# Performance work log

Hardware: AMD Instinct MI355X
Metric: run time of the kernel (lower is better)

Reference implementation:

```python
import jax, jax.numpy as jnp
import numpy as np

B_, S_, H_, O_ = 4, 2048, 2048, 2048
E_, R_ = 8, 16
LORA_ALPHA = 16.0


def setup_inputs() -> dict:
    key = jax.random.key(0)
    ks = jax.random.split(key, 5)
    x = jax.random.normal(ks[0], (B_, S_, H_), dtype=jnp.float32)
    W = jax.random.normal(ks[1], (O_, H_), dtype=jnp.float32) * 0.02   # frozen base weight [out, in]
    gate_w = jax.random.normal(ks[2], (E_, H_), dtype=jnp.float32) * 0.02  # router Linear weight [E, H]
    A = jax.random.normal(ks[3], (E_, R_, H_), dtype=jnp.float32) * 0.02   # stacked lora_A weights [E, r, in]
    B = jax.random.normal(ks[4], (E_, O_, R_), dtype=jnp.float32) * 0.02   # stacked lora_B weights [E, out, r]
    return {"x": x, "W": W, "gate_w": gate_w, "A": A, "B": B}


def reference(x, W, gate_w, A, B):
    bsz, seq, hid = x.shape
    E = gate_w.shape[0]
    x_flat = x.reshape(-1, hid)                                  # [T, H]

    # base linear
    out = x_flat @ W.T                                           # [T, O]

    # learned router: softmax -> top-2 -> renormalize
    logits = x_flat @ gate_w.T                                   # [T, E]
    probs = jax.nn.softmax(logits, axis=-1)
    topk_w, topk_idx = jax.lax.top_k(probs, 2)                   # [T, 2]
    topk_w = topk_w / jnp.sum(topk_w, axis=-1, keepdims=True)

    # per-token per-expert combine weight (sum over the 2 slots), scaled by alpha
    onehot = jax.nn.one_hot(topk_idx, E, dtype=x.dtype)          # [T, 2, E]
    wmat = jnp.einsum('tk,tke->te', topk_w, onehot) * LORA_ALPHA # [T, E]

    # dense grouped LoRA: h_e = x A_e^T ; out += sum_e w_te * (h_e B_e^T)
    h = jnp.einsum('th,erh->etr', x_flat, A)                     # [E, T, r]
    hw = h * wmat.T[:, :, None]                                  # [E, T, r]
    lora = jnp.einsum('etr,eor->to', hw, B)                      # [T, O]

    return (out + lora).reshape(bsz, seq, -1)
```

## Files before the change

### kernel.cpp

```cpp
#include <hip/hip_runtime.h>
#include <hip/hip_bf16.h>
#include <stdint.h>

#define T_TOK 8192
#define HID   2048
#define OUTD  2048
#define NE    8
#define RR    16
#define KAUG  2176
#define NH    128

typedef __bf16 bf16x8 __attribute__((ext_vector_type(8)));
typedef float  f32x4  __attribute__((ext_vector_type(4)));

#define AS1(p) ((__attribute__((address_space(1))) void*)(p))
#define AS3(p) ((__attribute__((address_space(3))) void*)(p))

__device__ inline unsigned short f2bf(float f) {
  unsigned int u = __builtin_bit_cast(unsigned int, f);
  unsigned int r = (u + 0x7fffu + ((u >> 16) & 1u)) >> 16;
  return (unsigned short)r;
}

__device__ inline ushort4 f2bf4(float4 v) {
  ushort4 u;
  u.x = f2bf(v.x); u.y = f2bf(v.y); u.z = f2bf(v.z); u.w = f2bf(v.w);
  return u;
}

__global__ __launch_bounds__(512) void k_prep(const float* __restrict__ x,
                                              const float* __restrict__ gw,
                                              const float* __restrict__ W,
                                              const float* __restrict__ Bw,
                                              const float* __restrict__ A,
                                              unsigned short* __restrict__ Xa,
                                              float* __restrict__ wte,
                                              unsigned short* __restrict__ Wa,
                                              unsigned short* __restrict__ Ag) {
  __shared__ float gws[NE * HID];
  if (blockIdx.x < 1024) {
#pragma unroll
    for (int i = 0; i < 8; ++i) {
      int idx = (i * 512 + (int)threadIdx.x) * 4;
      *(float4*)(gws + idx) = *(const float4*)(gw + idx);
    }
    __syncthreads();
    int w = threadIdx.x >> 6, lane = threadIdx.x & 63;
    int t = blockIdx.x * 8 + w;
    const float* xt = x + (size_t)t * HID;
    unsigned short* xo = Xa + (size_t)t * KAUG;
    double acc[8] = {0, 0, 0, 0, 0, 0, 0, 0};
#pragma unroll
    for (int i = 0; i < 8; ++i) {
      int k = (i * 64 + lane) * 4;
      float4 xv = *(const float4*)(xt + k);
      *(ushort4*)(xo + k) = f2bf4(xv);
#pragma unroll
      for (int e = 0; e < 8; ++e) {
        float4 gv = *(const float4*)(gws + e * HID + k);
        acc[e] += (double)xv.x * gv.x + (double)xv.y * gv.y +
                  (double)xv.z * gv.z + (double)xv.w * gv.w;
      }
    }
#pragma unroll
    for (int off = 32; off >= 1; off >>= 1)
#pragma unroll
      for (int e = 0; e < 8; ++e)
        acc[e] += __shfl_down(acc[e], off, 64);
    if (lane == 0) {
      int e0 = 0; double l0 = acc[0];
#pragma unroll
      for (int e = 1; e < 8; ++e) if (acc[e] > l0) { l0 = acc[e]; e0 = e; }
      int e1 = -1; double l1 = -1e300;
#pragma unroll
      for (int e = 0; e < 8; ++e) if (e != e0 && acc[e] > l1) { l1 = acc[e]; e1 = e; }
      double w0 = 16.0 / (1.0 + exp(l1 - l0));
      float o[8] = {0.f, 0.f, 0.f, 0.f, 0.f, 0.f, 0.f, 0.f};
      o[e0] = (float)w0;
      o[e1] = (float)(16.0 - w0);
      float4* p = (float4*)(wte + (size_t)t * 8);
      p[0] = make_float4(o[0], o[1], o[2], o[3]);
      p[1] = make_float4(o[4], o[5], o[6], o[7]);
    }
  } else {
    int b2 = blockIdx.x - 1024;
    if (b2 < 2048) {
      int tid = b2 * 512 + threadIdx.x;
      int row = tid >> 9, c = (tid & 511) << 2;
      float4 v = *(const float4*)(W + (size_t)row * HID + c);
      *(ushort4*)(Wa + (size_t)row * KAUG + c) = f2bf4(v);
    } else if (b2 < 2176) {
      int tid = (b2 - 2048) * 512 + threadIdx.x;
      int o = tid >> 5, j = (tid & 31) << 2;
      int e = j >> 4, r = j & 15;
      float4 v = *(const float4*)(Bw + (size_t)e * OUTD * RR + (size_t)o * RR + r);
      *(ushort4*)(Wa + (size_t)o * KAUG + 2048 + j) = f2bf4(v);
    } else {
      int tid = (b2 - 2176) * 512 + threadIdx.x;
      float4 v = *(const float4*)(A + (size_t)tid * 4);
      *(ushort4*)(Ag + (size_t)tid * 4) = f2bf4(v);
    }
  }
}

__global__ __launch_bounds__(256) void k_ha(const unsigned short* __restrict__ Xa,
                                            const unsigned short* __restrict__ Ag,
                                            const float* __restrict__ wte,
                                            unsigned short* __restrict__ XaW) {
  __shared__ unsigned short Xs[4][32 * 64];
  __shared__ unsigned short As[4][64 * 64];
  int tm = (blockIdx.x >> 1) * 32;
  int ch = (blockIdx.x & 1) * 64;
  int w = threadIdx.x >> 6, lane = threadIdx.x & 63;
  int lrow = lane >> 3;
  int lcol_s = (lane & 7) << 3;
  int lcol_g = ((lane & 7) ^ (lrow & 7)) << 3;

  const unsigned short* gX = Xa + (size_t)(tm + w * 8 + lrow) * KAUG + lcol_g;
  const unsigned short* gA = Ag + (size_t)(ch + w * 16 + lrow) * HID + lcol_g;
  int sxo = (w * 8 + lrow) * 64 + lcol_s;
  int sao = (w * 16 + lrow) * 64 + lcol_s;

  f32x4 acc[2] = {};

#define HA_STAGE(slot, koff) do {                                                         \
    __builtin_amdgcn_global_load_lds(AS1(gX + (koff)), AS3(&Xs[slot][0] + sxo), 16, 0, 0);\
    __builtin_amdgcn_global_load_lds(AS1(gA + (koff)), AS3(&As[slot][0] + sao), 16, 0, 0);\
    __builtin_amdgcn_global_load_lds(AS1(gA + (size_t)8 * HID + (koff)),                  \
                                     AS3(&As[slot][0] + 8 * 64 + sao), 16, 0, 0);         \
  } while (0)

#define HA_COMP(s) do {                                                                   \
    _Pragma("unroll")                                                                     \
    for (int ks = 0; ks < 2; ++ks) {                                                      \
      int kch = ks * 4 + (lane >> 4);                                                     \
      int ko = ((kch ^ (lane & 7)) << 3);                       \
      bf16x8 a = *(const bf16x8*)(&Xs[s][0] + ((w >> 1) * 16 + (lane & 15)) * 64 + ko);   \
      _Pragma("unroll")                                                                   \
      for (int fn = 0; fn < 2; ++fn) {                                                    \
        bf16x8 bv = *(const bf16x8*)(&As[s][0] + ((w & 1) * 32 + fn * 16 + (lane & 15)) * 64 + ko); \
        acc[fn] = __builtin_amdgcn_mfma_f32_16x16x32_bf16(a, bv, acc[fn], 0, 0, 0);       \
      }                                                                                   \
    }                                                                                     \
  } while (0)

  HA_STAGE(0, 0);
  HA_STAGE(1, 64);
  HA_STAGE(2, 128);
  for (int t = 0; t < 29; ++t) {
    asm volatile("s_waitcnt vmcnt(6)" ::: "memory");
    __builtin_amdgcn_s_barrier();
    HA_COMP(t & 3);
    __builtin_amdgcn_s_barrier();
    HA_STAGE((t + 3) & 3, (t + 3) * 64);
  }
  asm volatile("s_waitcnt vmcnt(6)" ::: "memory");
  __builtin_amdgcn_s_barrier();
  HA_COMP(1);
  asm volatile("s_waitcnt vmcnt(3)" ::: "memory");
  __builtin_amdgcn_s_barrier();
  HA_COMP(2);
  asm volatile("s_waitcnt vmcnt(0)" ::: "memory");
  __builtin_amdgcn_s_barrier();
  HA_COMP(3);
#undef HA_STAGE
#undef HA_COMP

  int q = lane >> 4;
#pragma unroll
  for (int fn = 0; fn < 2; ++fn) {
    int col = ch + (w & 1) * 32 + fn * 16 + (lane & 15);
    int e = col >> 4;
#pragma unroll
    for (int r = 0; r < 4; ++r) {
      int t = tm + (w >> 1) * 16 + q * 4 + r;
      float we = wte[(size_t)t * 8 + e];
      XaW[(size_t)t * KAUG + 2048 + col] = f2bf(we * acc[fn][r]);
    }
  }
}

__global__ __launch_bounds__(256, 4) void k_gemm(const unsigned short* __restrict__ Xa,
                                                 const unsigned short* __restrict__ Wa,
                                                 float* __restrict__ out) {
  __shared__ unsigned short As[128 * 64];
  __shared__ unsigned short Bs[128 * 64];
  int lid = blockIdx.x;
  int xcd = lid & 7, s = lid >> 3;
  int bm = (xcd * 8 + (s & 7)) * 128;
  int bn = (s >> 3) * 128;
  int w = threadIdx.x >> 6, lane = threadIdx.x & 63;
  int wm = (w >> 1) * 64, wn = (w & 1) * 64;
  int lrow = lane >> 3;
  int lcol_s = (lane & 7) << 3;
  int lcol_g = ((lane & 7) ^ (lrow & 7)) << 3;

  const unsigned short* gA = Xa + (size_t)(bm + w * 32 + lrow) * KAUG + lcol_g;
  const unsigned short* gB = Wa + (size_t)(bn + w * 32 + lrow) * KAUG + lcol_g;
  unsigned short* sA = As + (w * 32 + lrow) * 64 + lcol_s;
  unsigned short* sB = Bs + (w * 32 + lrow) * 64 + lcol_s;

  f32x4 acc[4][4] = {};
  for (int kt = 0; kt < KAUG; kt += 64) {
#pragma unroll
    for (int i = 0; i < 4; ++i) {
      __builtin_amdgcn_global_load_lds(AS1(gA + (size_t)i * 8 * KAUG), AS3(sA + i * 8 * 64), 16, 0, 0);
      __builtin_amdgcn_global_load_lds(AS1(gB + (size_t)i * 8 * KAUG), AS3(sB + i * 8 * 64), 16, 0, 0);
    }
    __syncthreads();
#pragma unroll
    for (int ks = 0; ks < 2; ++ks) {
      int kch = ks * 4 + (lane >> 4);
      int ko = ((kch ^ (lane & 7)) << 3);
      bf16x8 a[4], b[4];
#pragma unroll
      for (int f = 0; f < 4; ++f) a[f] = *(const bf16x8*)(As + (wm + f * 16 + (lane & 15)) * 64 + ko);
#pragma unroll
      for (int f = 0; f < 4; ++f) b[f] = *(const bf16x8*)(Bs + (wn + f * 16 + (lane & 15)) * 64 + ko);
#pragma unroll
      for (int fm = 0; fm < 4; ++fm)
#pragma unroll
        for (int fn = 0; fn < 4; ++fn)
          acc[fm][fn] = __builtin_amdgcn_mfma_f32_16x16x32_bf16(a[fm], b[fn], acc[fm][fn], 0, 0, 0);
    }
    __syncthreads();
    gA += 64; gB += 64;
  }
#pragma unroll
  for (int fm = 0; fm < 4; ++fm) {
    int row = bm + wm + fm * 16 + ((lane >> 4) << 2);
#pragma unroll
    for (int r = 0; r < 4; ++r) {
      float* orow = out + (size_t)(row + r) * OUTD + bn + wn + (lane & 15);
#pragma unroll
      for (int fn = 0; fn < 4; ++fn) orow[fn * 16] = acc[fm][fn][r];
    }
  }
}

extern "C" void kernel_launch(void* const* d_in, const int* in_sizes, int n_in,
                              void* d_out, int out_size, void* d_ws, size_t ws_size,
                              hipStream_t stream) {
  const float* x  = (const float*)d_in[0];
  const float* W  = (const float*)d_in[1];
  const float* gw = (const float*)d_in[2];
  const float* A  = (const float*)d_in[3];
  const float* B  = (const float*)d_in[4];
  float* out = (float*)d_out;

  char* ws = (char*)d_ws;
  unsigned short* Xa  = (unsigned short*)(ws);
  unsigned short* Wa  = (unsigned short*)(ws + 35651584);
  unsigned short* Ag  = (unsigned short*)(ws + 44564480);
  float*          wte = (float*)        (ws + 45088768);

  k_prep<<<3328, 512, 0, stream>>>(x, gw, W, B, A, Xa, wte, Wa, Ag);
  k_ha  <<<512, 256, 0, stream>>>(Xa, Ag, wte, Xa);
  k_gemm<<<1024, 256, 0, stream>>>(Xa, Wa, out);
}
```

Before: 220.7 us.

## Move weight conversion into k_ha and widen its blocks to cover all LoRA columns

The W and B fp32-to-bf16 conversion blocks move out of k_prep and into k_ha as extra blocks, so the weight conversion runs alongside the LoRA-A projection instead of before it. k_ha now uses 512-thread blocks that each compute all 128 expert-rank columns for a 32-token tile. This halves the number of times the X tile is loaded and drops the duplicated X loads. The per-wave vmcnt waits are adjusted because only four of the eight waves load X. The cost is more LDS per block and a larger, mixed-role grid for k_ha.

```diff
diff --git a/kernel.cpp b/kernel.cpp
--- a/kernel.cpp
+++ b/kernel.cpp
@@ -30,12 +30,9 @@
 
 __global__ __launch_bounds__(512) void k_prep(const float* __restrict__ x,
                                               const float* __restrict__ gw,
-                                              const float* __restrict__ W,
-                                              const float* __restrict__ Bw,
                                               const float* __restrict__ A,
                                               unsigned short* __restrict__ Xa,
                                               float* __restrict__ wte,
-                                              unsigned short* __restrict__ Wa,
                                               unsigned short* __restrict__ Ag) {
   __shared__ float gws[NE * HID];
   if (blockIdx.x < 1024) {
@@ -83,81 +80,91 @@
       p[1] = make_float4(o[4], o[5], o[6], o[7]);
     }
   } else {
-    int b2 = blockIdx.x - 1024;
+    int tid = (blockIdx.x - 1024) * 512 + threadIdx.x;
+    float4 v = *(const float4*)(A + (size_t)tid * 4);
+    *(ushort4*)(Ag + (size_t)tid * 4) = f2bf4(v);
+  }
+}
+
+__global__ __launch_bounds__(512) void k_ha(const unsigned short* __restrict__ Xa,
+                                            const unsigned short* __restrict__ Ag,
+                                            const float* __restrict__ wte,
+                                            unsigned short* __restrict__ XaW,
+                                            const float* __restrict__ W,
+                                            const float* __restrict__ Bw,
+                                            unsigned short* __restrict__ Wa) {
+  __shared__ unsigned short Xs[4][32 * 64];
+  __shared__ unsigned short As[4][128 * 64];
+  if (blockIdx.x >= 256) {
+    int b2 = blockIdx.x - 256;
     if (b2 < 2048) {
       int tid = b2 * 512 + threadIdx.x;
       int row = tid >> 9, c = (tid & 511) << 2;
       float4 v = *(const float4*)(W + (size_t)row * HID + c);
       *(ushort4*)(Wa + (size_t)row * KAUG + c) = f2bf4(v);
-    } else if (b2 < 2176) {
+    } else {
       int tid = (b2 - 2048) * 512 + threadIdx.x;
       int o = tid >> 5, j = (tid & 31) << 2;
       int e = j >> 4, r = j & 15;
       float4 v = *(const float4*)(Bw + (size_t)e * OUTD * RR + (size_t)o * RR + r);
       *(ushort4*)(Wa + (size_t)o * KAUG + 2048 + j) = f2bf4(v);
-    } else {
-      int tid = (b2 - 2176) * 512 + threadIdx.x;
-      float4 v = *(const float4*)(A + (size_t)tid * 4);
-      *(ushort4*)(Ag + (size_t)tid * 4) = f2bf4(v);
-    }
-  }
-}
-
-__global__ __launch_bounds__(256) void k_ha(const unsigned short* __restrict__ Xa,
-                                            const unsigned short* __restrict__ Ag,
-                                            const float* __restrict__ wte,
-                                            unsigned short* __restrict__ XaW) {
-  __shared__ unsigned short Xs[4][32 * 64];
-  __shared__ unsigned short As[4][64 * 64];
-  int tm = (blockIdx.x >> 1) * 32;
-  int ch = (blockIdx.x & 1) * 64;
+    }
+    return;
+  }
+
+  int tm = blockIdx.x * 32;
   int w = threadIdx.x >> 6, lane = threadIdx.x & 63;
+  int wm = (w >> 2) * 16, wn = (w & 3) * 32;
   int lrow = lane >> 3;
   int lcol_s = (lane & 7) << 3;
   int lcol_g = ((lane & 7) ^ (lrow & 7)) << 3;
 
-  const unsigned short* gX = Xa + (size_t)(tm + w * 8 + lrow) * KAUG + lcol_g;
-  const unsigned short* gA = Ag + (size_t)(ch + w * 16 + lrow) * HID + lcol_g;
-  int sxo = (w * 8 + lrow) * 64 + lcol_s;
+  const unsigned short* gX = Xa + (size_t)(tm + (w & 3) * 8 + lrow) * KAUG + lcol_g;
+  const unsigned short* gA = Ag + (size_t)(w * 16 + lrow) * HID + lcol_g;
+  int sxo = ((w & 3) * 8 + lrow) * 64 + lcol_s;
   int sao = (w * 16 + lrow) * 64 + lcol_s;
 
   f32x4 acc[2] = {};
 
-#define HA_STAGE(slot, koff) do {                                                         \
-    __builtin_amdgcn_global_load_lds(AS1(gX + (koff)), AS3(&Xs[slot][0] + sxo), 16, 0, 0);\
-    __builtin_amdgcn_global_load_lds(AS1(gA + (koff)), AS3(&As[slot][0] + sao), 16, 0, 0);\
-    __builtin_amdgcn_global_load_lds(AS1(gA + (size_t)8 * HID + (koff)),                  \
-                                     AS3(&As[slot][0] + 8 * 64 + sao), 16, 0, 0);         \
+#define HA_STAGE(slot, koff) do {                                                           \
+    if (w < 4)                                                                              \
+      __builtin_amdgcn_global_load_lds(AS1(gX + (koff)), AS3(&Xs[slot][0] + sxo), 16, 0, 0);\
+    __builtin_amdgcn_global_load_lds(AS1(gA + (koff)), AS3(&As[slot][0] + sao), 16, 0, 0);  \
+    __builtin_amdgcn_global_load_lds(AS1(gA + (size_t)8 * HID + (koff)),                    \
+                                     AS3(&As[slot][0] + 8 * 64 + sao), 16, 0, 0);           \
   } while (0)
 
-#define HA_COMP(s) do {                                                                   \
-    _Pragma("unroll")                                                                     \
-    for (int ks = 0; ks < 2; ++ks) {                                                      \
-      int kch = ks * 4 + (lane >> 4);                                                     \
-      int ko = ((kch ^ (lane & 7)) << 3);                       \
-      bf16x8 a = *(const bf16x8*)(&Xs[s][0] + ((w >> 1) * 16 + (lane & 15)) * 64 + ko);   \
-      _Pragma("unroll")                                                                   \
-      for (int fn = 0; fn < 2; ++fn) {                                                    \
-        bf16x8 bv = *(const bf16x8*)(&As[s][0] + ((w & 1) * 32 + fn * 16 + (lane & 15)) * 64 + ko); \
-        acc[fn] = __builtin_amdgcn_mfma_f32_16x16x32_bf16(a, bv, acc[fn], 0, 0, 0);       \
-      }                                                                                   \
-    }                                                                                     \
+#define HA_COMP(s) do {                                                                     \
+    _Pragma("unroll")                                                                       \
+    for (int ks = 0; ks < 2; ++ks) {                                                        \
+      int kch = ks * 4 + (lane >> 4);                                                       \
+      int ko = ((kch ^ (lane & 7)) << 3);                         \
+      bf16x8 a = *(const bf16x8*)(&Xs[s][0] + (wm + (lane & 15)) * 64 + ko);                \
+      _Pragma("unroll")                                                                     \
+      for (int fn = 0; fn < 2; ++fn) {                                                      \
+        bf16x8 bv = *(const bf16x8*)(&As[s][0] + (wn + fn * 16 + (lane & 15)) * 64 + ko);   \
+        acc[fn] = __builtin_amdgcn_mfma_f32_16x16x32_bf16(a, bv, acc[fn], 0, 0, 0);         \
+      }                                                                                     \
+    }                                                                                       \
   } while (0)
 
   HA_STAGE(0, 0);
   HA_STAGE(1, 64);
   HA_STAGE(2, 128);
   for (int t = 0; t < 29; ++t) {
-    asm volatile("s_waitcnt vmcnt(6)" ::: "memory");
+    if (w < 4) asm volatile("s_waitcnt vmcnt(6)" ::: "memory");
+    else       asm volatile("s_waitcnt vmcnt(4)" ::: "memory");
     __builtin_amdgcn_s_barrier();
     HA_COMP(t & 3);
     __builtin_amdgcn_s_barrier();
     HA_STAGE((t + 3) & 3, (t + 3) * 64);
   }
-  asm volatile("s_waitcnt vmcnt(6)" ::: "memory");
+  if (w < 4) asm volatile("s_waitcnt vmcnt(6)" ::: "memory");
+  else       asm volatile("s_waitcnt vmcnt(4)" ::: "memory");
   __builtin_amdgcn_s_barrier();
   HA_COMP(1);
-  asm volatile("s_waitcnt vmcnt(3)" ::: "memory");
+  if (w < 4) asm volatile("s_waitcnt vmcnt(3)" ::: "memory");
+  else       asm volatile("s_waitcnt vmcnt(2)" ::: "memory");
   __builtin_amdgcn_s_barrier();
   HA_COMP(2);
   asm volatile("s_waitcnt vmcnt(0)" ::: "memory");
@@ -169,11 +176,11 @@
   int q = lane >> 4;
 #pragma unroll
   for (int fn = 0; fn < 2; ++fn) {
-    int col = ch + (w & 1) * 32 + fn * 16 + (lane & 15);
+    int col = wn + fn * 16 + (lane & 15);
     int e = col >> 4;
 #pragma unroll
     for (int r = 0; r < 4; ++r) {
-      int t = tm + (w >> 1) * 16 + q * 4 + r;
+      int t = tm + wm + q * 4 + r;
       float we = wte[(size_t)t * 8 + e];
       XaW[(size_t)t * KAUG + 2048 + col] = f2bf(we * acc[fn][r]);
     }
@@ -254,7 +261,7 @@
   unsigned short* Ag  = (unsigned short*)(ws + 44564480);
   float*          wte = (float*)        (ws + 45088768);
 
-  k_prep<<<3328, 512, 0, stream>>>(x, gw, W, B, A, Xa, wte, Wa, Ag);
-  k_ha  <<<512, 256, 0, stream>>>(Xa, Ag, wte, Xa);
+  k_prep<<<1152, 512, 0, stream>>>(x, gw, A, Xa, wte, Ag);
+  k_ha  <<<2432, 512, 0, stream>>>(Xa, Ag, wte, Xa, W, B, Wa);
   k_gemm<<<1024, 256, 0, stream>>>(Xa, Wa, out);
 }
```

Result: slower. 227.4 us (+3.0%).

## Use 256x256 double-buffered GEMM tile with 512 threads and MFMA priority

Applied to the files above, without the earlier changes.

Replaces the 128x128 single-buffered main GEMM with a 256x256 tile computed by 8 waves, each owning a 128x64 sub-tile. LDS is double-buffered, so global-to-LDS loads for the next K-step run while the current step computes. s_setprio is raised around the MFMA blocks. The goal is more operand reuse per byte loaded and hidden load latency. The cost is 128 KB of LDS and 128 accumulator registers per lane, which limits occupancy to one block per CU, and the grid shrinks to 256 blocks.

```diff
diff --git a/kernel.cpp b/kernel.cpp
--- a/kernel.cpp
+++ b/kernel.cpp
@@ -9,6 +9,7 @@
 #define RR    16
 #define KAUG  2176
 #define NH    128
+#define NKT   34
 
 typedef __bf16 bf16x8 __attribute__((ext_vector_type(8)));
 typedef float  f32x4  __attribute__((ext_vector_type(4)));
@@ -134,7 +135,7 @@
     _Pragma("unroll")                                                                     \
     for (int ks = 0; ks < 2; ++ks) {                                                      \
       int kch = ks * 4 + (lane >> 4);                                                     \
-      int ko = ((kch ^ (lane & 7)) << 3);                       \
+      int ko = ((kch ^ (lane & 7)) << 3);                                                 \
       bf16x8 a = *(const bf16x8*)(&Xs[s][0] + ((w >> 1) * 16 + (lane & 15)) * 64 + ko);   \
       _Pragma("unroll")                                                                   \
       for (int fn = 0; fn < 2; ++fn) {                                                    \
@@ -180,60 +181,91 @@
   }
 }
 
-__global__ __launch_bounds__(256, 4) void k_gemm(const unsigned short* __restrict__ Xa,
+__global__ __launch_bounds__(512) void k_gemm256(const unsigned short* __restrict__ Xa,
                                                  const unsigned short* __restrict__ Wa,
                                                  float* __restrict__ out) {
-  __shared__ unsigned short As[128 * 64];
-  __shared__ unsigned short Bs[128 * 64];
-  int lid = blockIdx.x;
-  int xcd = lid & 7, s = lid >> 3;
-  int bm = (xcd * 8 + (s & 7)) * 128;
-  int bn = (s >> 3) * 128;
+  __shared__ unsigned short Asl[2][256 * 64];
+  __shared__ unsigned short Bsl[2][256 * 64];
+  int bid = blockIdx.x;
+  int xcd = bid & 7, idx = bid >> 3;
+  int bm = (xcd * 4 + (idx >> 3)) * 256;
+  int bn = (idx & 7) * 256;
   int w = threadIdx.x >> 6, lane = threadIdx.x & 63;
-  int wm = (w >> 1) * 64, wn = (w & 1) * 64;
+  int wm = (w >> 2) * 128;
+  int wn = (w & 3) * 64;
   int lrow = lane >> 3;
   int lcol_s = (lane & 7) << 3;
   int lcol_g = ((lane & 7) ^ (lrow & 7)) << 3;
 
-  const unsigned short* gA = Xa + (size_t)(bm + w * 32 + lrow) * KAUG + lcol_g;
-  const unsigned short* gB = Wa + (size_t)(bn + w * 32 + lrow) * KAUG + lcol_g;
-  unsigned short* sA = As + (w * 32 + lrow) * 64 + lcol_s;
-  unsigned short* sB = Bs + (w * 32 + lrow) * 64 + lcol_s;
-
-  f32x4 acc[4][4] = {};
-  for (int kt = 0; kt < KAUG; kt += 64) {
-#pragma unroll
-    for (int i = 0; i < 4; ++i) {
-      __builtin_amdgcn_global_load_lds(AS1(gA + (size_t)i * 8 * KAUG), AS3(sA + i * 8 * 64), 16, 0, 0);
-      __builtin_amdgcn_global_load_lds(AS1(gB + (size_t)i * 8 * KAUG), AS3(sB + i * 8 * 64), 16, 0, 0);
-    }
-    __syncthreads();
-#pragma unroll
-    for (int ks = 0; ks < 2; ++ks) {
-      int kch = ks * 4 + (lane >> 4);
-      int ko = ((kch ^ (lane & 7)) << 3);
-      bf16x8 a[4], b[4];
-#pragma unroll
-      for (int f = 0; f < 4; ++f) a[f] = *(const bf16x8*)(As + (wm + f * 16 + (lane & 15)) * 64 + ko);
-#pragma unroll
-      for (int f = 0; f < 4; ++f) b[f] = *(const bf16x8*)(Bs + (wn + f * 16 + (lane & 15)) * 64 + ko);
-#pragma unroll
-      for (int fm = 0; fm < 4; ++fm)
-#pragma unroll
-        for (int fn = 0; fn < 4; ++fn)
-          acc[fm][fn] = __builtin_amdgcn_mfma_f32_16x16x32_bf16(a[fm], b[fn], acc[fm][fn], 0, 0, 0);
-    }
-    __syncthreads();
-    gA += 64; gB += 64;
-  }
-#pragma unroll
-  for (int fm = 0; fm < 4; ++fm) {
-    int row = bm + wm + fm * 16 + ((lane >> 4) << 2);
+  const unsigned short* gA = Xa + (size_t)(bm + w * 8 + lrow) * KAUG + lcol_g;
+  const unsigned short* gB = Wa + (size_t)(bn + w * 8 + lrow) * KAUG + lcol_g;
+  int sO = (w * 8 + lrow) * 64 + lcol_s;
+
+#define G_STAGE(p, kt) do {                                                        \
+    _Pragma("unroll")                                                              \
+    for (int i = 0; i < 4; ++i) {                                                  \
+      __builtin_amdgcn_global_load_lds(AS1(gA + (size_t)i * 64 * KAUG + (kt) * 64),\
+                                       AS3(&Asl[p][0] + sO + i * 64 * 64), 16, 0, 0); \
+      __builtin_amdgcn_global_load_lds(AS1(gB + (size_t)i * 64 * KAUG + (kt) * 64),\
+                                       AS3(&Bsl[p][0] + sO + i * 64 * 64), 16, 0, 0); \
+    }                                                                              \
+  } while (0)
+
+  f32x4 acc[8][4] = {};
+
+#define G_COMP(p) do {                                                             \
+    __builtin_amdgcn_s_setprio(1);                                                 \
+    _Pragma("unroll")                                                              \
+    for (int kk = 0; kk < 2; ++kk) {                                               \
+      int kch = kk * 4 + (lane >> 4);                                              \
+      int ko = ((kch ^ (lane & 7)) << 3);                                          \
+      bf16x8 b[4];                                                                 \
+      _Pragma("unroll")                                                            \
+      for (int n = 0; n < 4; ++n)                                                  \
+        b[n] = *(const bf16x8*)(&Bsl[p][0] + (wn + n * 16 + (lane & 15)) * 64 + ko); \
+      _Pragma("unroll")                                                            \
+      for (int f = 0; f < 8; ++f) {                                                \
+        bf16x8 a = *(const bf16x8*)(&Asl[p][0] + (wm + f * 16 + (lane & 15)) * 64 + ko); \
+        _Pragma("unroll")                                                          \
+        for (int n = 0; n < 4; ++n)                                                \
+          acc[f][n] = __builtin_amdgcn_mfma_f32_16x16x32_bf16(a, b[n], acc[f][n], 0, 0, 0); \
+      }                                                                            \
+    }                                                                              \
+    __builtin_amdgcn_s_setprio(0);                                                 \
+  } while (0)
+
+  G_STAGE(0, 0);
+  G_STAGE(1, 1);
+  for (int kt = 0; kt < 32; kt += 2) {
+    asm volatile("s_waitcnt vmcnt(8)" ::: "memory");
+    __builtin_amdgcn_s_barrier();
+    G_COMP(0);
+    __builtin_amdgcn_s_barrier();
+    if (kt + 2 < NKT) G_STAGE(0, kt + 2);
+    asm volatile("s_waitcnt vmcnt(8)" ::: "memory");
+    __builtin_amdgcn_s_barrier();
+    G_COMP(1);
+    __builtin_amdgcn_s_barrier();
+    if (kt + 3 < NKT) G_STAGE(1, kt + 3);
+  }
+  asm volatile("s_waitcnt vmcnt(8)" ::: "memory");
+  __builtin_amdgcn_s_barrier();
+  G_COMP(0);
+  __builtin_amdgcn_s_barrier();
+  asm volatile("s_waitcnt vmcnt(0)" ::: "memory");
+  __builtin_amdgcn_s_barrier();
+  G_COMP(1);
+#undef G_STAGE
+#undef G_COMP
+
+#pragma unroll
+  for (int f = 0; f < 8; ++f) {
+    int row = bm + wm + f * 16 + ((lane >> 4) << 2);
 #pragma unroll
     for (int r = 0; r < 4; ++r) {
       float* orow = out + (size_t)(row + r) * OUTD + bn + wn + (lane & 15);
 #pragma unroll
-      for (int fn = 0; fn < 4; ++fn) orow[fn * 16] = acc[fm][fn][r];
+      for (int n = 0; n < 4; ++n) orow[n * 16] = acc[f][n][r];
     }
   }
 }
@@ -254,7 +286,7 @@
   unsigned short* Ag  = (unsigned short*)(ws + 44564480);
   float*          wte = (float*)        (ws + 45088768);
 
-  k_prep<<<3328, 512, 0, stream>>>(x, gw, W, B, A, Xa, wte, Wa, Ag);
-  k_ha  <<<512, 256, 0, stream>>>(Xa, Ag, wte, Xa);
-  k_gemm<<<1024, 256, 0, stream>>>(Xa, Wa, out);
-}
+  k_prep   <<<3328, 512, 0, stream>>>(x, gw, W, B, A, Xa, wte, Wa, Ag);
+  k_ha     <<<512, 256, 0, stream>>>(Xa, Ag, wte, Xa);
+  k_gemm256<<<256, 512, 0, stream>>>(Xa, Wa, out);
+}
```

Result: no change. 218.7 us (-0.9%).
